# Kernel optimization log

Hardware: AMD Instinct MI355X
Metric: run time of the kernel (lower is better)

The kernel has to match this reference:

```python
import jax, jax.numpy as jnp
import numpy as np

EPS = 1e-5  # nn.BatchNorm1d default eps


def setup_inputs() -> dict:
    key = jax.random.key(0)
    ks = jax.random.split(key, 8)
    N_NODES, N_EDGES = 50000, 800000
    D_NODE, D_EDGE, HID, NCLS = 128, 64, 256, 8
    D_IN = D_EDGE + 2 * D_NODE  # 320
    return {
        "n_feats": jax.random.normal(ks[0], (N_NODES, D_NODE), dtype=jnp.float32),
        "edge_feats": jax.random.normal(ks[1], (N_EDGES, D_EDGE), dtype=jnp.float32),
        "src_idx": jax.random.randint(ks[2], (N_EDGES,), 0, N_NODES, dtype=jnp.int64),
        "dst_idx": jax.random.randint(ks[3], (N_EDGES,), 0, N_NODES, dtype=jnp.int64),
        "W1": jax.random.normal(ks[4], (HID, D_IN), dtype=jnp.float32) * (1.0 / np.sqrt(D_IN)),
        "b1": jnp.zeros((HID,), dtype=jnp.float32),
        "gamma": jnp.ones((HID,), dtype=jnp.float32),
        "beta": jnp.zeros((HID,), dtype=jnp.float32),
        "W2": jax.random.normal(ks[5], (NCLS, HID), dtype=jnp.float32) * (1.0 / np.sqrt(HID)),
        "b2": jnp.zeros((NCLS,), dtype=jnp.float32),
    }


def reference(n_feats, edge_feats, src_idx, dst_idx, W1, b1, gamma, beta, W2, b2):
    # gather-concat: [E, d_edge + 2*d_node]
    h = jnp.concatenate([edge_feats, n_feats[src_idx], n_feats[dst_idx]], axis=1)
    # Linear 1
    z = jnp.einsum("ei,hi->eh", h, W1) + b1
    # BatchNorm1d in training mode: batch mean / biased variance over edges
    mu = jnp.mean(z, axis=0)
    var = jnp.mean(jnp.square(z - mu), axis=0)
    zn = (z - mu) * jax.lax.rsqrt(var + EPS) * gamma + beta
    # Linear 2 + LogSoftmax(dim=1)
    logits = jnp.einsum("eh,ch->ec", zn, W2) + b2
    return jax.nn.log_softmax(logits, axis=1)
```

## Files before the change

kernel.cpp:

```cpp
#include <hip/hip_runtime.h>
#include <hip/hip_bf16.h>


#define N_EDGES 800000
#define N_NODES 50000

typedef __attribute__((ext_vector_type(8))) short short8;
typedef __attribute__((ext_vector_type(4))) float f32x4;

#define WS_SUM   0
#define WS_SQ    16384
#define WS_CVEC  32768
#define WS_FLAG  32832
#define WS_MBIG  33280
#define WS_MB    43520
#define WS_MF    45568
#define WS_W1B   55808
#define WS_PS    262144
#define WS_PD    2097152
#define WS_NFB   4194304
#define WS_FAST_NEED (4u << 20)
#define WS_BIG_NEED  16994304u

__device__ __forceinline__ ushort f2bf(float f) {
    union { float f; unsigned int u; } x; x.f = f;
    unsigned int r = x.u + 0x7FFFu + ((x.u >> 16) & 1u);
    return (ushort)(r >> 16);
}
__device__ __forceinline__ short8 cvt8(const float* __restrict__ p) {
    short8 r;
    #pragma unroll
    for (int i = 0; i < 8; i++) r[i] = (short)f2bf(p[i]);
    return r;
}
__device__ __forceinline__ short8 cvtpair(uint4 a, uint4 b) {
    unsigned int v[8] = {a.x, a.y, a.z, a.w, b.x, b.y, b.z, b.w};
    short8 r;
    #pragma unroll
    for (int i = 0; i < 8; i++) {
        unsigned int u = v[i];
        unsigned int rr = u + 0x7FFFu + ((u >> 16) & 1u);
        r[i] = (short)(rr >> 16);
    }
    return r;
}

__device__ __forceinline__ int aidx(int s, int r, int c) {
    return ((s * 128 + r) * 4 + (c ^ ((r >> 1) & 3))) * 8;
}

__global__ void detect_kernel(const int* __restrict__ src,
                              const int* __restrict__ dst, int* flag) {
    int t = threadIdx.x;
    int v = src[2 * t + 1] | dst[2 * t + 1];
    #pragma unroll
    for (int o = 32; o >= 1; o >>= 1) v |= __shfl_xor(v, o);
    if (t == 0) *flag = (v == 0) ? 1 : 0;
}

__global__ __launch_bounds__(256) void prep_kernel(const float* __restrict__ W1,
                                                   ushort* __restrict__ W1b) {
    const int i = (blockIdx.x * 256 + threadIdx.x) * 4;
    const float4 v = *(const float4*)(W1 + i);
    ushort4 o;
    o.x = f2bf(v.x); o.y = f2bf(v.y); o.z = f2bf(v.z); o.w = f2bf(v.w);
    *(ushort4*)(W1b + i) = o;
}

__global__ __launch_bounds__(256) void prep_all_kernel(
    const float* __restrict__ nf, const float* __restrict__ W1,
    const int* __restrict__ src, const int* __restrict__ dst,
    ushort* __restrict__ nfb, ushort* __restrict__ W1b,
    float* __restrict__ zreg, int* __restrict__ flag)
{
    const int t = threadIdx.x;
    const int b = blockIdx.x;
    if (b < 3125) {
        const long i = (long)b * 2048 + t * 8;
        const float4 v0 = *(const float4*)(nf + i);
        const float4 v1 = *(const float4*)(nf + i + 4);
        short8 o;
        o[0] = (short)f2bf(v0.x); o[1] = (short)f2bf(v0.y);
        o[2] = (short)f2bf(v0.z); o[3] = (short)f2bf(v0.w);
        o[4] = (short)f2bf(v1.x); o[5] = (short)f2bf(v1.y);
        o[6] = (short)f2bf(v1.z); o[7] = (short)f2bf(v1.w);
        *(short8*)(nfb + i) = o;
    } else if (b < 3205) {
        const int i = (b - 3125) * 1024 + t * 4;
        const float4 v = *(const float4*)(W1 + i);
        ushort4 o;
        o.x = f2bf(v.x); o.y = f2bf(v.y); o.z = f2bf(v.z); o.w = f2bf(v.w);
        *(ushort4*)(W1b + i) = o;
    } else {
        for (int i = t; i < 8320; i += 256) zreg[i] = 0.f;
        __syncthreads();
        if (t < 64) {
            int v = src[2 * t + 1] | dst[2 * t + 1];
            #pragma unroll
            for (int o = 32; o >= 1; o >>= 1) v |= __shfl_xor(v, o);
            if (t == 0) *flag = (v == 0) ? 1 : 0;
        }
    }
}

template <bool NFB>
__global__ __launch_bounds__(512, 4) void gemm1_stats_kernel(
    const float* __restrict__ nf, const ushort* __restrict__ nfb,
    const float* __restrict__ ef,
    const int* __restrict__ src, const int* __restrict__ dst,
    const ushort* __restrict__ W1b, const int* __restrict__ flag,
    float* __restrict__ g_sum, float* __restrict__ g_sq)
{
    __shared__ ushort a_lds[10 * 128 * 32];

    const int t    = threadIdx.x;
    const int lane = t & 63;
    const int wave = t >> 6;
    const int quad = lane >> 4;
    const int l15  = lane & 15;

    const int wide = *flag;
    const int r     = t >> 2;
    const int chunk = t & 3;
    const long e   = (long)blockIdx.x * 128 + r;
    const int si = src[e << wide], di = dst[e << wide];
    const float* pe = ef + e * 64;

    uint4 efu[2][2];
    #pragma unroll
    for (int s = 0; s < 2; s++) {
        const float* p = pe + s * 32 + chunk * 8;
        efu[s][0] = *(const uint4*)p;
        efu[s][1] = *(const uint4*)(p + 4);
    }

    const ushort* wbase = W1b + (wave * 32 + l15) * 320 + quad * 8;
    short8 bpre[3][2];
    #pragma unroll
    for (int in = 0; in < 2; in++)
        bpre[0][in] = *(const short8*)(wbase + in * 16 * 320);
    #pragma unroll
    for (int in = 0; in < 2; in++)
        bpre[1][in] = *(const short8*)(wbase + in * 16 * 320 + 32);

    if constexpr (NFB) {
        const ushort* psb = nfb + (long)si * 128 + chunk * 8;
        const ushort* pdb = nfb + (long)di * 128 + chunk * 8;
        short8 g[8];
        #pragma unroll
        for (int i = 0; i < 4; i++) g[i]     = *(const short8*)(psb + i * 32);
        #pragma unroll
        for (int i = 0; i < 4; i++) g[4 + i] = *(const short8*)(pdb + i * 32);
        #pragma unroll
        for (int s = 0; s < 2; s++)
            *(short8*)&a_lds[aidx(s, r, chunk)] = cvtpair(efu[s][0], efu[s][1]);
        #pragma unroll
        for (int i = 0; i < 8; i++)
            *(short8*)&a_lds[aidx(2 + i, r, chunk)] = g[i];
    } else {
        const float* ps = nf + (long)si * 128 + chunk * 8;
        const float* pd = nf + (long)di * 128 + chunk * 8;
        uint4 pn[16];
        #pragma unroll
        for (int i = 0; i < 4; i++) {
            pn[i * 2]     = *(const uint4*)(ps + i * 32);
            pn[i * 2 + 1] = *(const uint4*)(ps + i * 32 + 4);
        }
        #pragma unroll
        for (int i = 0; i < 4; i++) {
            pn[8 + i * 2]     = *(const uint4*)(pd + i * 32);
            pn[8 + i * 2 + 1] = *(const uint4*)(pd + i * 32 + 4);
        }
        #pragma unroll
        for (int s = 0; s < 2; s++)
            *(short8*)&a_lds[aidx(s, r, chunk)] = cvtpair(efu[s][0], efu[s][1]);
        #pragma unroll
        for (int i = 0; i < 8; i++)
            *(short8*)&a_lds[aidx(2 + i, r, chunk)] =
                cvtpair(pn[i * 2], pn[i * 2 + 1]);
    }
    __syncthreads();

    f32x4 acc[8][2];
    #pragma unroll
    for (int mb = 0; mb < 8; mb++)
        #pragma unroll
        for (int in = 0; in < 2; in++)
            acc[mb][in] = (f32x4){0.f, 0.f, 0.f, 0.f};

    #pragma unroll
    for (int ks = 0; ks < 10; ks++) {
        if (ks < 8) {
            #pragma unroll
            for (int in = 0; in < 2; in++)
                bpre[(ks + 2) % 3][in] =
                    *(const short8*)(wbase + in * 16 * 320 + (ks + 2) * 32);
        }
        __builtin_amdgcn_s_setprio(1);
        #pragma unroll
        for (int mb = 0; mb < 8; mb++) {
            short8 afr = *(const short8*)
                &a_lds[aidx(ks, mb * 16 + l15, quad)];
            #pragma unroll
            for (int in = 0; in < 2; in++)
                acc[mb][in] = __builtin_amdgcn_mfma_f32_16x16x32_bf16(
                    afr, bpre[ks % 3][in], acc[mb][in], 0, 0, 0);
        }
        __builtin_amdgcn_s_setprio(0);
    }

    const int slot = blockIdx.x & 15;
    #pragma unroll
    for (int in = 0; in < 2; in++) {
        const int col = wave * 32 + in * 16 + l15;
        float s = 0.f, q = 0.f;
        #pragma unroll
        for (int mb = 0; mb < 8; mb++)
            #pragma unroll
            for (int j = 0; j < 4; j++) {
                float v = acc[mb][in][j];
                s += v; q += v * v;
            }
        s += __shfl_xor(s, 16); s += __shfl_xor(s, 32);
        q += __shfl_xor(q, 16); q += __shfl_xor(q, 32);
        if (quad == 0) {
            atomicAdd(&g_sum[slot * 256 + col], s);
            atomicAdd(&g_sq[slot * 256 + col], q);
        }
    }
}

__global__ __launch_bounds__(256) void fold_kernel(
    const float* __restrict__ gamma, const float* __restrict__ beta,
    const float* __restrict__ W1, const float* __restrict__ b1,
    const float* __restrict__ W2, const float* __restrict__ b2,
    const float* __restrict__ g_sum, const float* __restrict__ g_sq,
    ushort* __restrict__ Mbig, ushort* __restrict__ Mb,
    float* __restrict__ Mf, float* __restrict__ Cvec)
{
    __shared__ float a_sh[256][8];
    __shared__ float red[8];
    __shared__ float mk_sh[64][8];
    const int t = threadIdx.x;

    float ssum = 0.f, ssq = 0.f;
    #pragma unroll
    for (int s = 0; s < 16; s++) {
        ssum += g_sum[s * 256 + t];
        ssq  += g_sq[s * 256 + t];
    }
    const float invE   = 1.0f / (float)N_EDGES;
    const float mu_acc = ssum * invE;
    float var = ssq * invE - mu_acc * mu_acc;
    var = fmaxf(var, 0.f);
    const float b1v = b1[t];
    const float mu  = mu_acc + b1v;
    const float g   = gamma[t] * rsqrtf(var + 1e-5f);
    const float sh  = b1v * g + beta[t] - mu * g;

    if (t < 8) red[t] = 0.f;
    ((float*)mk_sh)[t] = 0.f;
    ((float*)mk_sh)[t + 256] = 0.f;
    __syncthreads();
    #pragma unroll
    for (int c = 0; c < 8; c++) {
        const float w = W2[c * 256 + t];
        a_sh[t][c] = w * g;
        if (blockIdx.x == 0) atomicAdd(&red[c], w * sh);
    }
    __syncthreads();

    const int k  = blockIdx.x * 64 + (t & 63);
    const int q4 = t >> 6;
    float m[8] = {0.f, 0.f, 0.f, 0.f, 0.f, 0.f, 0.f, 0.f};
    #pragma unroll 8
    for (int hh = q4 * 64; hh < q4 * 64 + 64; hh++) {
        const float w1 = W1[hh * 320 + k];
        #pragma unroll
        for (int c = 0; c < 8; c++) m[c] += a_sh[hh][c] * w1;
    }
    #pragma unroll
    for (int c = 0; c < 8; c++) atomicAdd(&mk_sh[t & 63][c], m[c]);
    __syncthreads();

    if (t < 64) {
        const int kk = blockIdx.x * 64 + t;
        #pragma unroll
        for (int c = 0; c < 8; c++) {
            const float mv = mk_sh[t][c];
            Mf[c * 320 + kk]   = mv;
            Mbig[c * 320 + kk] = f2bf(mv);
            if (kk < 64) Mb[c * 64 + kk] = f2bf(mv);
        }
        #pragma unroll
        for (int c = 8; c < 16; c++) {
            Mbig[c * 320 + kk] = 0;
            if (kk < 64) Mb[c * 64 + kk] = 0;
        }
    }
    if (blockIdx.x == 0) {
        if (t < 8)       Cvec[t] = b2[t] + red[t];
        else if (t < 16) Cvec[t] = 0.f;
    }
}

__global__ __launch_bounds__(256) void fold_nodeproj_kernel(
    const float* __restrict__ gamma, const float* __restrict__ beta,
    const float* __restrict__ W1, const float* __restrict__ b1,
    const float* __restrict__ W2, const float* __restrict__ b2,
    const float* __restrict__ g_sum, const float* __restrict__ g_sq,
    const float* __restrict__ nf, ushort* __restrict__ Mb,
    float* __restrict__ Cvec, float* __restrict__ Ps, float* __restrict__ Pd)
{
    __shared__ float a_sh[256][8];
    __shared__ float red[8];
    __shared__ float Ms[8][128];
    __shared__ float Md[8][128];
    const int t = threadIdx.x;

    float ssum = 0.f, ssq = 0.f;
    #pragma unroll
    for (int s = 0; s < 16; s++) {
        ssum += g_sum[s * 256 + t];
        ssq  += g_sq[s * 256 + t];
    }
    const float invE   = 1.0f / (float)N_EDGES;
    const float mu_acc = ssum * invE;
    float var = ssq * invE - mu_acc * mu_acc;
    var = fmaxf(var, 0.f);
    const float b1v = b1[t];
    const float mu  = mu_acc + b1v;
    const float g   = gamma[t] * rsqrtf(var + 1e-5f);
    const float sh  = b1v * g + beta[t] - mu * g;

    if (t < 8) red[t] = 0.f;
    __syncthreads();
    #pragma unroll
    for (int c = 0; c < 8; c++) {
        const float w = W2[c * 256 + t];
        a_sh[t][c] = w * g;
        if (blockIdx.x == 0) atomicAdd(&red[c], w * sh);
    }
    __syncthreads();

    float m[8] = {0.f, 0.f, 0.f, 0.f, 0.f, 0.f, 0.f, 0.f};
    #pragma unroll 8
    for (int hh = 0; hh < 256; hh++) {
        const float w1 = W1[hh * 320 + 64 + t];
        #pragma unroll
        for (int c = 0; c < 8; c++) m[c] += a_sh[hh][c] * w1;
    }
    #pragma unroll
    for (int c = 0; c < 8; c++) {
        if (t < 128) Ms[c][t] = m[c];
        else         Md[c][t - 128] = m[c];
    }
    if (blockIdx.x == 0) {
        if (t < 64) {
            float mm[8] = {0.f, 0.f, 0.f, 0.f, 0.f, 0.f, 0.f, 0.f};
            #pragma unroll 8
            for (int hh = 0; hh < 256; hh++) {
                const float w1 = W1[hh * 320 + t];
                #pragma unroll
                for (int c = 0; c < 8; c++) mm[c] += a_sh[hh][c] * w1;
            }
            #pragma unroll
            for (int c = 0; c < 8; c++)  Mb[c * 64 + t] = f2bf(mm[c]);
            #pragma unroll
            for (int c = 8; c < 16; c++) Mb[c * 64 + t] = 0;
        }
        if (t < 8)       Cvec[t] = b2[t] + red[t];
        else if (t < 16) Cvec[t] = 0.f;
    }
    __syncthreads();

    const int n = blockIdx.x * 256 + t;
    if (n >= N_NODES) return;
    float as[8] = {0,0,0,0,0,0,0,0}, ad[8] = {0,0,0,0,0,0,0,0};
    #pragma unroll 4
    for (int k = 0; k < 128; k += 4) {
        const float4 v = *(const float4*)(nf + (long)n * 128 + k);
        #pragma unroll
        for (int c = 0; c < 8; c++) {
            const float4 ms = *(const float4*)&Ms[c][k];
            const float4 md = *(const float4*)&Md[c][k];
            as[c] += v.x * ms.x + v.y * ms.y + v.z * ms.z + v.w * ms.w;
            ad[c] += v.x * md.x + v.y * md.y + v.z * md.z + v.w * md.w;
        }
    }
    #pragma unroll
    for (int c = 0; c < 8; c++) {
        Ps[n * 8 + c] = as[c];
        Pd[n * 8 + c] = ad[c];
    }
}

__global__ __launch_bounds__(256) void nodeproj_kernel(
    const float* __restrict__ nf, const float* __restrict__ Mf,
    float* __restrict__ Ps, float* __restrict__ Pd)
{
    __shared__ float Ms[8][128];
    __shared__ float Md[8][128];
    const int t = threadIdx.x;
    #pragma unroll
    for (int i = 0; i < 4; i++) {
        const int f = t + i * 256;
        Ms[f >> 7][f & 127] = Mf[(f >> 7) * 320 + 64  + (f & 127)];
        Md[f >> 7][f & 127] = Mf[(f >> 7) * 320 + 192 + (f & 127)];
    }
    __syncthreads();
    const int n = blockIdx.x * 256 + t;
    if (n >= N_NODES) return;
    float as[8] = {0,0,0,0,0,0,0,0}, ad[8] = {0,0,0,0,0,0,0,0};
    #pragma unroll 4
    for (int k = 0; k < 128; k += 4) {
        const float4 v = *(const float4*)(nf + (long)n * 128 + k);
        #pragma unroll
        for (int c = 0; c < 8; c++) {
            const float4 ms = *(const float4*)&Ms[c][k];
            const float4 md = *(const float4*)&Md[c][k];
            as[c] += v.x * ms.x + v.y * ms.y + v.z * ms.z + v.w * ms.w;
            ad[c] += v.x * md.x + v.y * md.y + v.z * md.z + v.w * md.w;
        }
    }
    #pragma unroll
    for (int c = 0; c < 8; c++) {
        Ps[n * 8 + c] = as[c];
        Pd[n * 8 + c] = ad[c];
    }
}

__global__ __launch_bounds__(256) void edge_out_kernel(
    const float* __restrict__ ef, const int* __restrict__ src,
    const int* __restrict__ dst, const int* __restrict__ flag,
    const ushort* __restrict__ Mb, const float* __restrict__ Ps,
    const float* __restrict__ Pd, const float* __restrict__ Cvec,
    float* __restrict__ out)
{
    __shared__ float x_sh[4][64][20];
    const int t    = threadIdx.x;
    const int lane = t & 63;
    const int wave = t >> 6;
    const int quad = lane >> 4;
    const int l15  = lane & 15;
    const int wide = *flag;
    const long eb  = (long)blockIdx.x * 256 + wave * 64;

    const long ei = (eb + lane) << wide;
    const int sidx = src[ei], didx = dst[ei];
    const float4 s0 = *(const float4*)(Ps + sidx * 8);
    const float4 s1 = *(const float4*)(Ps + sidx * 8 + 4);
    const float4 d0 = *(const float4*)(Pd + didx * 8);
    const float4 d1 = *(const float4*)(Pd + didx * 8 + 4);
    const float4 c0 = *(const float4*)(Cvec);
    const float4 c1 = *(const float4*)(Cvec + 4);

    uint4 ea[4][2], eb4[4][2];
    #pragma unroll
    for (int mb = 0; mb < 4; mb++)
        #pragma unroll
        for (int ks = 0; ks < 2; ks++) {
            const float* p = ef + (eb + mb * 16 + l15) * 64 + ks * 32 + quad * 8;
            ea[mb][ks]  = *(const uint4*)p;
            eb4[mb][ks] = *(const uint4*)(p + 4);
        }

    f32x4 acc[4];
    #pragma unroll
    for (int mb = 0; mb < 4; mb++) acc[mb] = (f32x4){0.f, 0.f, 0.f, 0.f};

    const ushort* bbase = Mb + l15 * 64 + quad * 8;
    #pragma unroll
    for (int ks = 0; ks < 2; ks++) {
        short8 bfr = *(const short8*)(bbase + ks * 32);
        #pragma unroll
        for (int mb = 0; mb < 4; mb++)
            acc[mb] = __builtin_amdgcn_mfma_f32_16x16x32_bf16(
                cvtpair(ea[mb][ks], eb4[mb][ks]), bfr, acc[mb], 0, 0, 0);
    }

    #pragma unroll
    for (int mb = 0; mb < 4; mb++)
        #pragma unroll
        for (int j = 0; j < 4; j++)
            x_sh[wave][mb * 16 + quad * 4 + j][l15] = acc[mb][j];
    __syncthreads();

    const float4 xa = *(const float4*)&x_sh[wave][lane][0];
    const float4 xb = *(const float4*)&x_sh[wave][lane][4];

    float x0 = xa.x + c0.x + s0.x + d0.x;
    float x1 = xa.y + c0.y + s0.y + d0.y;
    float x2 = xa.z + c0.z + s0.z + d0.z;
    float x3 = xa.w + c0.w + s0.w + d0.w;
    float x4 = xb.x + c1.x + s1.x + d1.x;
    float x5 = xb.y + c1.y + s1.y + d1.y;
    float x6 = xb.z + c1.z + s1.z + d1.z;
    float x7 = xb.w + c1.w + s1.w + d1.w;

    float m = fmaxf(fmaxf(fmaxf(x0, x1), fmaxf(x2, x3)),
                    fmaxf(fmaxf(x4, x5), fmaxf(x6, x7)));
    float sx = __expf(x0 - m) + __expf(x1 - m) + __expf(x2 - m) +
               __expf(x3 - m) + __expf(x4 - m) + __expf(x5 - m) +
               __expf(x6 - m) + __expf(x7 - m);
    const float l = m + __logf(sx);

    float* po = out + (eb + lane) * 8;
    float4 o0 = {x0 - l, x1 - l, x2 - l, x3 - l};
    float4 o1 = {x4 - l, x5 - l, x6 - l, x7 - l};
    *(float4*)po       = o0;
    *(float4*)(po + 4) = o1;
}

__global__ __launch_bounds__(256) void out_kernel(
    const float* __restrict__ nf, const float* __restrict__ ef,
    const int* __restrict__ src, const int* __restrict__ dst,
    const int* __restrict__ flag, const ushort* __restrict__ M,
    const float* __restrict__ Cvec, float* __restrict__ out)
{
    const int t    = threadIdx.x;
    const int lane = t & 63;
    const int wave = t >> 6;
    const int quad = lane >> 4;
    const int l15  = lane & 15;
    const int wide = *flag;
    const long eb  = (long)blockIdx.x * 256 + wave * 64;

    const float* pe[4]; const float* ps[4]; const float* pd[4];
    #pragma unroll
    for (int mb = 0; mb < 4; mb++) {
        const long e  = eb + mb * 16 + l15;
        const int si = src[e << wide], di = dst[e << wide];
        pe[mb] = ef + e * 64;
        ps[mb] = nf + (long)si * 128;
        pd[mb] = nf + (long)di * 128;
    }
    f32x4 acc[4];
    #pragma unroll
    for (int mb = 0; mb < 4; mb++) acc[mb] = (f32x4){0.f, 0.f, 0.f, 0.f};
    const ushort* bbase = M + l15 * 320 + quad * 8;
    #pragma unroll
    for (int ks = 0; ks < 10; ks++) {
        const int k0 = ks * 32;
        short8 bfr = *(const short8*)(bbase + k0);
        const int koff = k0 + quad * 8;
        #pragma unroll
        for (int mb = 0; mb < 4; mb++) {
            const float* p = (ks < 2) ? (pe[mb] + koff)
                           : (ks < 6) ? (ps[mb] + (koff - 64))
                                      : (pd[mb] + (koff - 192));
            acc[mb] = __builtin_amdgcn_mfma_f32_16x16x32_bf16(
                cvt8(p), bfr, acc[mb], 0, 0, 0);
        }
    }
    const float bv = Cvec[l15];
    #pragma unroll
    for (int mb = 0; mb < 4; mb++)
        #pragma unroll
        for (int j = 0; j < 4; j++) {
            float x = acc[mb][j] + bv;
            float m = x;
            m = fmaxf(m, __shfl_xor(m, 1));
            m = fmaxf(m, __shfl_xor(m, 2));
            m = fmaxf(m, __shfl_xor(m, 4));
            float sx = __expf(x - m);
            sx += __shfl_xor(sx, 1);
            sx += __shfl_xor(sx, 2);
            sx += __shfl_xor(sx, 4);
            const float o = x - m - __logf(sx);
            if (l15 < 8)
                out[(eb + mb * 16 + quad * 4 + j) * 8 + l15] = o;
        }
}

extern "C" void kernel_launch(void* const* d_in, const int* in_sizes, int n_in,
                              void* d_out, int out_size, void* d_ws, size_t ws_size,
                              hipStream_t stream) {
    const float* nf    = (const float*)d_in[0];
    const float* ef    = (const float*)d_in[1];
    const int*   src   = (const int*)d_in[2];
    const int*   dst   = (const int*)d_in[3];
    const float* W1    = (const float*)d_in[4];
    const float* b1    = (const float*)d_in[5];
    const float* gamma = (const float*)d_in[6];
    const float* beta  = (const float*)d_in[7];
    const float* W2    = (const float*)d_in[8];
    const float* b2    = (const float*)d_in[9];

    char*   ws    = (char*)d_ws;
    float*  g_sum = (float*)(ws + WS_SUM);
    float*  g_sq  = (float*)(ws + WS_SQ);
    float*  Cvec  = (float*)(ws + WS_CVEC);
    int*    flag  = (int*)(ws + WS_FLAG);
    ushort* Mbig  = (ushort*)(ws + WS_MBIG);
    ushort* Mb    = (ushort*)(ws + WS_MB);
    float*  Mf    = (float*)(ws + WS_MF);
    ushort* W1b   = (ushort*)(ws + WS_W1B);
    float*  Ps    = (float*)(ws + WS_PS);
    float*  Pd    = (float*)(ws + WS_PD);
    ushort* nfb   = (ushort*)(ws + WS_NFB);
    float*  out   = (float*)d_out;

    const bool fast = ws_size >= (size_t)WS_FAST_NEED;
    const bool big  = ws_size >= (size_t)WS_BIG_NEED;

    if (big) {
        prep_all_kernel<<<3206, 256, 0, stream>>>(nf, W1, src, dst, nfb, W1b,
                                                  (float*)ws, flag);
        gemm1_stats_kernel<true><<<N_EDGES / 128, 512, 0, stream>>>(
            nf, nfb, ef, src, dst, W1b, flag, g_sum, g_sq);
        fold_nodeproj_kernel<<<(N_NODES + 255) / 256, 256, 0, stream>>>(
            gamma, beta, W1, b1, W2, b2, g_sum, g_sq, nf, Mb, Cvec, Ps, Pd);
        edge_out_kernel<<<N_EDGES / 256, 256, 0, stream>>>(ef, src, dst, flag,
                                                           Mb, Ps, Pd, Cvec, out);
    } else {
        hipMemsetAsync(ws, 0, 33280, stream);
        detect_kernel<<<1, 64, 0, stream>>>(src, dst, flag);
        prep_kernel<<<80, 256, 0, stream>>>(W1, W1b);
        gemm1_stats_kernel<false><<<N_EDGES / 128, 512, 0, stream>>>(
            nf, nfb, ef, src, dst, W1b, flag, g_sum, g_sq);
        fold_kernel<<<5, 256, 0, stream>>>(gamma, beta, W1, b1, W2, b2,
                                           g_sum, g_sq, Mbig, Mb, Mf, Cvec);
        if (fast) {
            nodeproj_kernel<<<(N_NODES + 255) / 256, 256, 0, stream>>>(nf, Mf, Ps, Pd);
            edge_out_kernel<<<N_EDGES / 256, 256, 0, stream>>>(ef, src, dst, flag,
                                                               Mb, Ps, Pd, Cvec, out);
        } else {
            out_kernel<<<N_EDGES / 256, 256, 0, stream>>>(nf, ef, src, dst, flag,
                                                          Mbig, Cvec, out);
        }
    }
}
```

Before: 516.2 us.

## Switch gemm1 stats kernel to 32x32x16 MFMA with 2x2 wave tiling

Replaces the per-wave 128x32 tile built from 16x16x32 MFMAs with a 64x64 tile per wave (two row halves by four column groups) using 32x32x16 bf16 MFMAs. Each wave now reads half as many A fragments from LDS and issues fewer, larger MFMAs, which reduces LDS traffic per flop. The K loop doubles to 20 steps of 16 and W1 prefetch is adapted to match. The column-statistics reduction is also reworked for the 32x32 accumulator layout. The cost is more accumulator registers per lane (64 floats) and a longer dependent chain of MFMAs per step.

After: 650.0 us. +25.9%, slower.

```diff
diff --git a/kernel.cpp b/kernel.cpp
--- a/kernel.cpp
+++ b/kernel.cpp
@@ -7,6 +7,7 @@
 
 typedef __attribute__((ext_vector_type(8))) short short8;
 typedef __attribute__((ext_vector_type(4))) float f32x4;
+typedef __attribute__((ext_vector_type(16))) float f32x16;
 
 #define WS_SUM   0
 #define WS_SQ    16384
@@ -116,8 +117,10 @@
     const int t    = threadIdx.x;
     const int lane = t & 63;
     const int wave = t >> 6;
-    const int quad = lane >> 4;
-    const int l15  = lane & 15;
+    const int l31  = lane & 31;
+    const int kh   = lane >> 5;
+    const int rh   = wave >> 2;
+    const int cg   = wave & 3;
 
     const int wide = *flag;
     const int r     = t >> 2;
@@ -134,14 +137,14 @@
         efu[s][1] = *(const uint4*)(p + 4);
     }
 
-    const ushort* wbase = W1b + (wave * 32 + l15) * 320 + quad * 8;
+    const ushort* wb0 = W1b + (cg * 64 + l31) * 320 + kh * 8;
+    const ushort* wb1 = wb0 + 32 * 320;
+
     short8 bpre[3][2];
-    #pragma unroll
-    for (int in = 0; in < 2; in++)
-        bpre[0][in] = *(const short8*)(wbase + in * 16 * 320);
-    #pragma unroll
-    for (int in = 0; in < 2; in++)
-        bpre[1][in] = *(const short8*)(wbase + in * 16 * 320 + 32);
+    bpre[0][0] = *(const short8*)(wb0);
+    bpre[0][1] = *(const short8*)(wb1);
+    bpre[1][0] = *(const short8*)(wb0 + 16);
+    bpre[1][1] = *(const short8*)(wb1 + 16);
 
     if constexpr (NFB) {
         const ushort* psb = nfb + (long)si * 128 + chunk * 8;
@@ -181,49 +184,53 @@
     }
     __syncthreads();
 
-    f32x4 acc[8][2];
-    #pragma unroll
-    for (int mb = 0; mb < 8; mb++)
-        #pragma unroll
-        for (int in = 0; in < 2; in++)
-            acc[mb][in] = (f32x4){0.f, 0.f, 0.f, 0.f};
-
-    #pragma unroll
-    for (int ks = 0; ks < 10; ks++) {
-        if (ks < 8) {
+    f32x16 acc[2][2];
+    #pragma unroll
+    for (int rt = 0; rt < 2; rt++)
+        #pragma unroll
+        for (int ct = 0; ct < 2; ct++)
             #pragma unroll
-            for (int in = 0; in < 2; in++)
-                bpre[(ks + 2) % 3][in] =
-                    *(const short8*)(wbase + in * 16 * 320 + (ks + 2) * 32);
-        }
+            for (int j = 0; j < 16; j++)
+                acc[rt][ct][j] = 0.f;
+
+    #pragma unroll
+    for (int kt = 0; kt < 20; kt++) {
+        if (kt < 18) {
+            bpre[(kt + 2) % 3][0] = *(const short8*)(wb0 + (kt + 2) * 16);
+            bpre[(kt + 2) % 3][1] = *(const short8*)(wb1 + (kt + 2) * 16);
+        }
+        const int s = kt >> 1, h = kt & 1;
+        short8 afr0 = *(const short8*)
+            &a_lds[aidx(s, rh * 64 + l31,      h * 2 + kh)];
+        short8 afr1 = *(const short8*)
+            &a_lds[aidx(s, rh * 64 + 32 + l31, h * 2 + kh)];
         __builtin_amdgcn_s_setprio(1);
-        #pragma unroll
-        for (int mb = 0; mb < 8; mb++) {
-            short8 afr = *(const short8*)
-                &a_lds[aidx(ks, mb * 16 + l15, quad)];
+        acc[0][0] = __builtin_amdgcn_mfma_f32_32x32x16_bf16(
+            afr0, bpre[kt % 3][0], acc[0][0], 0, 0, 0);
+        acc[0][1] = __builtin_amdgcn_mfma_f32_32x32x16_bf16(
+            afr0, bpre[kt % 3][1], acc[0][1], 0, 0, 0);
+        acc[1][0] = __builtin_amdgcn_mfma_f32_32x32x16_bf16(
+            afr1, bpre[kt % 3][0], acc[1][0], 0, 0, 0);
+        acc[1][1] = __builtin_amdgcn_mfma_f32_32x32x16_bf16(
+            afr1, bpre[kt % 3][1], acc[1][1], 0, 0, 0);
+        __builtin_amdgcn_s_setprio(0);
+    }
+
+    const int slot = blockIdx.x & 15;
+    #pragma unroll
+    for (int ct = 0; ct < 2; ct++) {
+        float s = 0.f, q = 0.f;
+        #pragma unroll
+        for (int rt = 0; rt < 2; rt++)
             #pragma unroll
-            for (int in = 0; in < 2; in++)
-                acc[mb][in] = __builtin_amdgcn_mfma_f32_16x16x32_bf16(
-                    afr, bpre[ks % 3][in], acc[mb][in], 0, 0, 0);
-        }
-        __builtin_amdgcn_s_setprio(0);
-    }
-
-    const int slot = blockIdx.x & 15;
-    #pragma unroll
-    for (int in = 0; in < 2; in++) {
-        const int col = wave * 32 + in * 16 + l15;
-        float s = 0.f, q = 0.f;
-        #pragma unroll
-        for (int mb = 0; mb < 8; mb++)
-            #pragma unroll
-            for (int j = 0; j < 4; j++) {
-                float v = acc[mb][in][j];
+            for (int j = 0; j < 16; j++) {
+                float v = acc[rt][ct][j];
                 s += v; q += v * v;
             }
-        s += __shfl_xor(s, 16); s += __shfl_xor(s, 32);
-        q += __shfl_xor(q, 16); q += __shfl_xor(q, 32);
-        if (quad == 0) {
+        s += __shfl_xor(s, 32);
+        q += __shfl_xor(q, 32);
+        if (lane < 32) {
+            const int col = cg * 64 + ct * 32 + l31;
             atomicAdd(&g_sum[slot * 256 + col], s);
             atomicAdd(&g_sq[slot * 256 + col], q);
         }
```
